# Optimization experiments

Measured on AMD Instinct MI355X. Metric: run time of the kernel, lower is better.

## Reference

```python
import jax, jax.numpy as jnp
import numpy as np
from jax import lax

B, C1, C2, OUT, H, W = 8, 256, 128, 256, 64, 64
MID = max(C1, C2)
D = max(MID // 8, 4)

def conv1x1(x, w, b=None):
    # x: [B,C,H,W], w: [O,C]
    y = jnp.einsum('bchw,oc->bohw', x, w)
    if b is not None:
        y = y + b[None, :, None, None]
    return y

def dwconv3x3(x, w, b):
    # depthwise 3x3, padding=1; w: [C,1,3,3]
    y = lax.conv_general_dilated(x, w, (1, 1), 'SAME',
                                 dimension_numbers=('NCHW', 'OIHW', 'NCHW'),
                                 feature_group_count=x.shape[1])
    return y + b[None, :, None, None]

def setup_inputs() -> dict:
    key = jax.random.key(0)
    ks = jax.random.split(key, 16)
    def w1x1(k, o, i):
        return jax.random.normal(k, (o, i), jnp.float32) * np.sqrt(2.0 / o)
    def wdw(k, c):
        return jax.random.normal(k, (c, 1, 3, 3), jnp.float32) * np.sqrt(2.0 / (9 * c))
    z = lambda c: jnp.zeros((c,), jnp.float32)
    return {
        'x1': jax.random.normal(ks[0], (B, C1, H, W), jnp.float32),
        'x2': jax.random.normal(ks[1], (B, C2, H, W), jnp.float32),
        'conv_r_w': w1x1(ks[2], MID, C1), 'conv_r_b': z(MID),
        'conv_n_w': w1x1(ks[3], MID, C2), 'conv_n_b': z(MID),
        'mlp_w1': w1x1(ks[4], D, MID),
        'mlp_w2': w1x1(ks[5], 2 * MID, D),
        'pq_w': w1x1(ks[6], MID, MID), 'pq_b': z(MID),
        'dq_w': wdw(ks[7], MID), 'dq_b': z(MID),
        'pk_w': w1x1(ks[8], MID, MID), 'pk_b': z(MID),
        'dk_w': wdw(ks[9], MID), 'dk_b': z(MID),
        'pv_w': w1x1(ks[10], MID, MID), 'pv_b': z(MID),
        'dv_w': wdw(ks[11], MID), 'dv_b': z(MID),
        'out_w': w1x1(ks[12], OUT, MID), 'out_b': z(OUT),
        'alpha': jnp.float32(1.0),
        'lambd': jnp.float32(0.5),
        'beta': jnp.float32(0.5),
    }

def reference(x1, x2, conv_r_w, conv_r_b, conv_n_w, conv_n_b, mlp_w1, mlp_w2,
              pq_w, pq_b, dq_w, dq_b, pk_w, pk_b, dk_w, dk_b,
              pv_w, pv_b, dv_w, dv_b, out_w, out_b, alpha, lambd, beta):
    FR = conv1x1(x1, conv_r_w, conv_r_b)          # [B,C,H,W]
    FN = conv1x1(x2, conv_n_w, conv_n_b)          # [B,C,H,W]
    stack = jnp.stack([FR, FN], axis=1)           # [B,2,C,H,W]
    feats_sum = FR + FN
    pooled = feats_sum.mean(axis=(2, 3))          # [B,C] (adaptive avg pool 1x1)
    h = jax.nn.relu(jnp.einsum('bc,dc->bd', pooled, mlp_w1))
    a = jnp.einsum('bd,ed->be', h, mlp_w2).reshape(B, 2, MID)
    attn = jax.nn.softmax(a, axis=1)              # softmax over the 2 branches
    Fw = jnp.einsum('bkchw,bkc->bchw', stack, attn)
    Q = dwconv3x3(conv1x1(Fw, pq_w, pq_b), dq_w, dq_b)
    K = dwconv3x3(conv1x1(Fw, pk_w, pk_b), dk_w, dk_b)
    V = dwconv3x3(conv1x1(Fw, pv_w, pv_b), dv_w, dv_b)
    FQ = jnp.fft.fft2(Q.astype(jnp.float32), axes=(-2, -1))   # complex64 [B,C,H,W]
    FK = jnp.fft.fft2(K.astype(jnp.float32), axes=(-2, -1))
    elem = (FQ * FK).reshape(B, MID, H * W)                    # [B,C,HW]
    FQf = FQ.reshape(B, MID, H * W)
    FKf = FK.reshape(B, MID, H * W)
    attn_matrix = jnp.einsum('bcn,bdn->bcd', FQf, FKf)         # complex [B,C,C]
    attn_w = jax.nn.softmax(jnp.abs(attn_matrix) / alpha, axis=-1)
    attn_wc = attn_w.astype(jnp.complex64)
    F_CFR = jnp.einsum('bcd,bdn->bcn', attn_wc, elem).reshape(B, MID, H, W)
    cfr = jnp.real(jnp.fft.ifft2(F_CFR, axes=(-2, -1))).astype(Q.dtype)
    F_DFR = V - lambd * V * cfr
    freq_out = Q * cfr + F_DFR
    output = beta * freq_out + (1.0 - beta) * Fw
    return conv1x1(output, out_w, out_b)
```

## Files before the change

kernel.cpp:

```cpp
#include <hip/hip_runtime.h>
#include <math.h>

#ifndef M_PI
#define M_PI 3.14159265358979323846
#endif

typedef unsigned int u32;

constexpr int  NB   = 8;
constexpr int  CH   = 256;
constexpr long HW   = 4096;
constexpr long SLOT = (long)NB * CH * HW;
constexpr int  SPLITK = 8;
constexpr long ST   = (long)CH * HW;

__device__ __forceinline__ float rne_hi(float x) {
  unsigned u = __float_as_uint(x);
  unsigned r = (u + 0x7FFFu + ((u >> 16) & 1u)) & 0xFFFF0000u;
  return __uint_as_float(r);
}
__device__ __forceinline__ u32 packf(float x) {
  const float h = rne_hi(x);
  const float l = x - h;
  return (__float_as_uint(h) & 0xFFFF0000u) | (__float_as_uint(l) >> 16);
}
__device__ __forceinline__ float unpackf(u32 u) {
  return __uint_as_float(u & 0xFFFF0000u) + __uint_as_float(u << 16);
}
__device__ __forceinline__ unsigned bfpair(float x, float y) {
  return (__float_as_uint(x) >> 16) | (__float_as_uint(y) & 0xFFFF0000u);
}

typedef short bf16x8 __attribute__((ext_vector_type(8)));
typedef float f32x4  __attribute__((ext_vector_type(4)));

__global__ __launch_bounds__(256)
void cvt_kernel(const float* __restrict__ src, u32* __restrict__ dst, int n4)
{
  const int i = blockIdx.x * 256 + threadIdx.x;
  if (i < n4) {
    const float4 v = ((const float4*)src)[i];
    uint4 o;
    o.x = packf(v.x); o.y = packf(v.y); o.z = packf(v.z); o.w = packf(v.w);
    ((uint4*)dst)[i] = o;
  }
}

template<bool BPACKED, int EPI>
__global__ __launch_bounds__(256)
void gemm_mfma(const u32* __restrict__ A, const void* __restrict__ Bv,
               void* __restrict__ Cv, const float* __restrict__ bias,
               int K, long aStride, long bStride, long cStride,
               const u32* __restrict__ qb, const u32* __restrict__ vb,
               const u32* __restrict__ fwb,
               const float* __restrict__ lambd, const float* __restrict__ beta)
{
  constexpr int N = 4096;
  __shared__ __align__(16) unsigned short sAh[128 * 48];
  __shared__ __align__(16) unsigned short sAl[128 * 48];
  __shared__ __align__(16) unsigned short sBh[128 * 48];
  __shared__ __align__(16) unsigned short sBl[128 * 48];

  const int tid = threadIdx.x;
  const int b   = blockIdx.z;
  const int m0  = blockIdx.y * 128;
  const int n0  = blockIdx.x * 128;
  const u32* Ab = A + (long)b * aStride;

  const int ar = tid >> 1;
  const int ak = (tid & 1) * 16;
  const int aBase = ar * 48 + ak;
  const int bn = tid & 127;
  const int bk = (tid >> 7) * 16;
  const int bBase = bn * 48 + bk;

  const int wv = tid >> 6, lane = tid & 63;
  const int wy = wv >> 1, wx = wv & 1;
  const int quad = lane >> 4, l15 = lane & 15;

  f32x4 acc[4][4];
#pragma unroll
  for (int i = 0; i < 4; ++i)
#pragma unroll
    for (int j = 0; j < 4; ++j) acc[i][j] = (f32x4){0.f, 0.f, 0.f, 0.f};

  u32   ra[16];
  u32   rbu[16];
  float rbf[16];
  {
    const u32* ap = Ab + (long)(m0 + ar) * K + ak;
#pragma unroll
    for (int i = 0; i < 4; ++i) {
      const uint4 t = *(const uint4*)(ap + i * 4);
      ra[4*i] = t.x; ra[4*i+1] = t.y; ra[4*i+2] = t.z; ra[4*i+3] = t.w;
    }
    if (BPACKED) {
      const u32* bp = (const u32*)Bv + (long)b * bStride + (long)bk * N + n0 + bn;
#pragma unroll
      for (int i = 0; i < 16; ++i) rbu[i] = bp[(long)i * N];
    } else {
      const float* bp = (const float*)Bv + (long)b * bStride + (long)bk * N + n0 + bn;
#pragma unroll
      for (int i = 0; i < 16; ++i) rbf[i] = bp[(long)i * N];
    }
  }

  for (int kt = 0; kt < K; kt += 32) {
    {
      u32 hi[8], lo[8];
#pragma unroll
      for (int e = 0; e < 8; ++e) {
        const u32 u0 = ra[2*e], u1 = ra[2*e+1];
        hi[e] = (u0 >> 16) | (u1 & 0xFFFF0000u);
        lo[e] = (u0 & 0xFFFFu) | (u1 << 16);
      }
      *(uint4*)&sAh[aBase]     = make_uint4(hi[0], hi[1], hi[2], hi[3]);
      *(uint4*)&sAh[aBase + 8] = make_uint4(hi[4], hi[5], hi[6], hi[7]);
      *(uint4*)&sAl[aBase]     = make_uint4(lo[0], lo[1], lo[2], lo[3]);
      *(uint4*)&sAl[aBase + 8] = make_uint4(lo[4], lo[5], lo[6], lo[7]);
    }
    if (BPACKED) {
      u32 hi[8], lo[8];
#pragma unroll
      for (int e = 0; e < 8; ++e) {
        const u32 u0 = rbu[2*e], u1 = rbu[2*e+1];
        hi[e] = (u0 >> 16) | (u1 & 0xFFFF0000u);
        lo[e] = (u0 & 0xFFFFu) | (u1 << 16);
      }
      *(uint4*)&sBh[bBase]     = make_uint4(hi[0], hi[1], hi[2], hi[3]);
      *(uint4*)&sBh[bBase + 8] = make_uint4(hi[4], hi[5], hi[6], hi[7]);
      *(uint4*)&sBl[bBase]     = make_uint4(lo[0], lo[1], lo[2], lo[3]);
      *(uint4*)&sBl[bBase + 8] = make_uint4(lo[4], lo[5], lo[6], lo[7]);
    } else {
      float h[16], l[16];
#pragma unroll
      for (int e = 0; e < 16; ++e) { h[e] = rne_hi(rbf[e]); l[e] = rbf[e] - h[e]; }
      *(uint4*)&sBh[bBase]     = make_uint4(bfpair(h[0],h[1]), bfpair(h[2],h[3]),
                                            bfpair(h[4],h[5]), bfpair(h[6],h[7]));
      *(uint4*)&sBh[bBase + 8] = make_uint4(bfpair(h[8],h[9]), bfpair(h[10],h[11]),
                                            bfpair(h[12],h[13]), bfpair(h[14],h[15]));
      *(uint4*)&sBl[bBase]     = make_uint4(bfpair(l[0],l[1]), bfpair(l[2],l[3]),
                                            bfpair(l[4],l[5]), bfpair(l[6],l[7]));
      *(uint4*)&sBl[bBase + 8] = make_uint4(bfpair(l[8],l[9]), bfpair(l[10],l[11]),
                                            bfpair(l[12],l[13]), bfpair(l[14],l[15]));
    }
    __syncthreads();

    if (kt + 32 < K) {
      const u32* ap = Ab + (long)(m0 + ar) * K + kt + 32 + ak;
#pragma unroll
      for (int i = 0; i < 4; ++i) {
        const uint4 t = *(const uint4*)(ap + i * 4);
        ra[4*i] = t.x; ra[4*i+1] = t.y; ra[4*i+2] = t.z; ra[4*i+3] = t.w;
      }
      if (BPACKED) {
        const u32* bp = (const u32*)Bv + (long)b * bStride + (long)(kt + 32 + bk) * N + n0 + bn;
#pragma unroll
        for (int i = 0; i < 16; ++i) rbu[i] = bp[(long)i * N];
      } else {
        const float* bp = (const float*)Bv + (long)b * bStride + (long)(kt + 32 + bk) * N + n0 + bn;
#pragma unroll
        for (int i = 0; i < 16; ++i) rbf[i] = bp[(long)i * N];
      }
    }

    bf16x8 ah[4], al[4];
#pragma unroll
    for (int i = 0; i < 4; ++i) {
      const int idx = (wy * 64 + i * 16 + l15) * 48 + quad * 8;
      ah[i] = *(const bf16x8*)&sAh[idx];
      al[i] = *(const bf16x8*)&sAl[idx];
    }
#pragma unroll
    for (int j = 0; j < 4; ++j) {
      const int idx = (wx * 64 + j * 16 + l15) * 48 + quad * 8;
      const bf16x8 bh = *(const bf16x8*)&sBh[idx];
      const bf16x8 bl = *(const bf16x8*)&sBl[idx];
#pragma unroll
      for (int i = 0; i < 4; ++i) {
        acc[i][j] = __builtin_amdgcn_mfma_f32_16x16x32_bf16(ah[i], bh, acc[i][j], 0, 0, 0);
        acc[i][j] = __builtin_amdgcn_mfma_f32_16x16x32_bf16(ah[i], bl, acc[i][j], 0, 0, 0);
        acc[i][j] = __builtin_amdgcn_mfma_f32_16x16x32_bf16(al[i], bh, acc[i][j], 0, 0, 0);
      }
    }
    __syncthreads();
  }

  if (EPI == 0) {
    float* Cb = (float*)Cv + (long)b * cStride;
#pragma unroll
    for (int i = 0; i < 4; ++i)
#pragma unroll
      for (int r = 0; r < 4; ++r) {
        const int row = m0 + wy * 64 + i * 16 + quad * 4 + r;
        const float bb = bias ? bias[row] : 0.f;
#pragma unroll
        for (int j = 0; j < 4; ++j) {
          const int col = n0 + wx * 64 + j * 16 + l15;
          Cb[(long)row * N + col] = acc[i][j][r] + bb;
        }
      }
  } else if (EPI == 1) {
    u32* Cb = (u32*)Cv + (long)b * cStride;
#pragma unroll
    for (int i = 0; i < 4; ++i)
#pragma unroll
      for (int r = 0; r < 4; ++r) {
        const int row = m0 + wy * 64 + i * 16 + quad * 4 + r;
        const float bb = bias ? bias[row] : 0.f;
#pragma unroll
        for (int j = 0; j < 4; ++j) {
          const int col = n0 + wx * 64 + j * 16 + l15;
          Cb[(long)row * N + col] = packf(acc[i][j][r] + bb);
        }
      }
  } else {
    u32* Cb = (u32*)Cv + (long)b * cStride;
    const float lam = lambd[0], bet = beta[0];
#pragma unroll
    for (int i = 0; i < 4; ++i)
#pragma unroll
      for (int r = 0; r < 4; ++r) {
        const int row = m0 + wy * 64 + i * 16 + quad * 4 + r;
#pragma unroll
        for (int j = 0; j < 4; ++j) {
          const int col = n0 + wx * 64 + j * 16 + l15;
          const long off = (long)row * N + col;
          const long gi  = (long)b * cStride + off;
          const float q = unpackf(qb[gi]);
          const float v = unpackf(vb[gi]);
          const float f = unpackf(fwb[gi]);
          Cb[off] = packf(bet * (acc[i][j][r] * (q - lam * v) + v) + (1.f - bet) * f);
        }
      }
  }
}

__global__ __launch_bounds__(256)
void gemm_logits(const u32* __restrict__ Q, const u32* __restrict__ Kr,
                 float* __restrict__ Lp)
{
  __shared__ __align__(16) unsigned short sAh[128 * 48];
  __shared__ __align__(16) unsigned short sAl[128 * 48];
  __shared__ __align__(16) unsigned short sBh[128 * 48];
  __shared__ __align__(16) unsigned short sBl[128 * 48];

  const int tid = threadIdx.x;
  const int bz  = blockIdx.z;
  const int b   = bz >> 3, sp = bz & 7;
  const int m0  = blockIdx.y * 128;
  const int n0  = blockIdx.x * 128;
  const long k0b = (long)sp * 512;

  const int ar = tid >> 1;
  const int ak = (tid & 1) * 16;
  const int aBase = ar * 48 + ak;

  const int wv = tid >> 6, lane = tid & 63;
  const int wy = wv >> 1, wx = wv & 1;
  const int quad = lane >> 4, l15 = lane & 15;

  f32x4 acc[4][4];
#pragma unroll
  for (int i = 0; i < 4; ++i)
#pragma unroll
    for (int j = 0; j < 4; ++j) acc[i][j] = (f32x4){0.f, 0.f, 0.f, 0.f};

  const u32* Abase = Q  + (long)b * ST + (long)(m0 + ar) * 4096 + k0b + ak;
  const u32* Bbase = Kr + (long)b * ST + (long)(n0 + ar) * 4096 + k0b + ak;

  u32 ra[16], rb[16];
#pragma unroll
  for (int i = 0; i < 4; ++i) {
    uint4 t = *(const uint4*)(Abase + i * 4);
    ra[4*i] = t.x; ra[4*i+1] = t.y; ra[4*i+2] = t.z; ra[4*i+3] = t.w;
    t = *(const uint4*)(Bbase + i * 4);
    rb[4*i] = t.x; rb[4*i+1] = t.y; rb[4*i+2] = t.z; rb[4*i+3] = t.w;
  }

  for (int kt = 0; kt < 512; kt += 32) {
    {
      u32 hi[8], lo[8];
#pragma unroll
      for (int e = 0; e < 8; ++e) {
        const u32 u0 = ra[2*e], u1 = ra[2*e+1];
        hi[e] = (u0 >> 16) | (u1 & 0xFFFF0000u);
        lo[e] = (u0 & 0xFFFFu) | (u1 << 16);
      }
      *(uint4*)&sAh[aBase]     = make_uint4(hi[0], hi[1], hi[2], hi[3]);
      *(uint4*)&sAh[aBase + 8] = make_uint4(hi[4], hi[5], hi[6], hi[7]);
      *(uint4*)&sAl[aBase]     = make_uint4(lo[0], lo[1], lo[2], lo[3]);
      *(uint4*)&sAl[aBase + 8] = make_uint4(lo[4], lo[5], lo[6], lo[7]);
#pragma unroll
      for (int e = 0; e < 8; ++e) {
        const u32 u0 = rb[2*e], u1 = rb[2*e+1];
        hi[e] = (u0 >> 16) | (u1 & 0xFFFF0000u);
        lo[e] = (u0 & 0xFFFFu) | (u1 << 16);
      }
      *(uint4*)&sBh[aBase]     = make_uint4(hi[0], hi[1], hi[2], hi[3]);
      *(uint4*)&sBh[aBase + 8] = make_uint4(hi[4], hi[5], hi[6], hi[7]);
      *(uint4*)&sBl[aBase]     = make_uint4(lo[0], lo[1], lo[2], lo[3]);
      *(uint4*)&sBl[aBase + 8] = make_uint4(lo[4], lo[5], lo[6], lo[7]);
    }
    __syncthreads();

    if (kt + 32 < 512) {
#pragma unroll
      for (int i = 0; i < 4; ++i) {
        uint4 t = *(const uint4*)(Abase + kt + 32 + i * 4);
        ra[4*i] = t.x; ra[4*i+1] = t.y; ra[4*i+2] = t.z; ra[4*i+3] = t.w;
        t = *(const uint4*)(Bbase + kt + 32 + i * 4);
        rb[4*i] = t.x; rb[4*i+1] = t.y; rb[4*i+2] = t.z; rb[4*i+3] = t.w;
      }
    }

    bf16x8 ah[4], al[4];
#pragma unroll
    for (int i = 0; i < 4; ++i) {
      const int idx = (wy * 64 + i * 16 + l15) * 48 + quad * 8;
      ah[i] = *(const bf16x8*)&sAh[idx];
      al[i] = *(const bf16x8*)&sAl[idx];
    }
#pragma unroll
    for (int j = 0; j < 4; ++j) {
      const int idx = (wx * 64 + j * 16 + l15) * 48 + quad * 8;
      const bf16x8 bh = *(const bf16x8*)&sBh[idx];
      const bf16x8 bl = *(const bf16x8*)&sBl[idx];
#pragma unroll
      for (int i = 0; i < 4; ++i) {
        acc[i][j] = __builtin_amdgcn_mfma_f32_16x16x32_bf16(ah[i], bh, acc[i][j], 0, 0, 0);
        acc[i][j] = __builtin_amdgcn_mfma_f32_16x16x32_bf16(ah[i], bl, acc[i][j], 0, 0, 0);
        acc[i][j] = __builtin_amdgcn_mfma_f32_16x16x32_bf16(al[i], bh, acc[i][j], 0, 0, 0);
      }
    }
    __syncthreads();
  }

  float* Lb = Lp + (long)bz * 65536;
#pragma unroll
  for (int i = 0; i < 4; ++i)
#pragma unroll
    for (int r = 0; r < 4; ++r) {
      const int row = m0 + wy * 64 + i * 16 + quad * 4 + r;
#pragma unroll
      for (int j = 0; j < 4; ++j) {
        const int col = n0 + wx * 64 + j * 16 + l15;
        Lb[(long)row * 256 + col] = acc[i][j][r];
      }
    }
}

__global__ __launch_bounds__(256)
void pool_kernel(const u32* __restrict__ FR, const u32* __restrict__ FN,
                 float* __restrict__ pooled)
{
  __shared__ float red[256];
  const int bc = blockIdx.x, tid = threadIdx.x;
  const uint4* a = (const uint4*)(FR + (long)bc * HW);
  const uint4* b = (const uint4*)(FN + (long)bc * HW);
  float s = 0.f;
  for (int v = tid; v < 1024; v += 256) {
    const uint4 x = a[v];
    s += unpackf(x.x) + unpackf(x.y) + unpackf(x.z) + unpackf(x.w);
    const uint4 y = b[v];
    s += unpackf(y.x) + unpackf(y.y) + unpackf(y.z) + unpackf(y.w);
  }
  red[tid] = s; __syncthreads();
  for (int o = 128; o > 0; o >>= 1) {
    if (tid < o) red[tid] += red[tid + o];
    __syncthreads();
  }
  if (tid == 0) pooled[bc] = red[0] * (1.f / 4096.f);
}

__global__ __launch_bounds__(256)
void attn2_kernel(const float* __restrict__ pooled, const float* __restrict__ w1,
                  const float* __restrict__ w2, float* __restrict__ attn2)
{
  __shared__ float ps[256];
  __shared__ float hs[32];
  const int b = blockIdx.x, tid = threadIdx.x;
  ps[tid] = pooled[b * 256 + tid];
  __syncthreads();
  if (tid < 32) {
    float a = 0.f;
    for (int c = 0; c < 256; ++c) a += ps[c] * w1[tid * 256 + c];
    hs[tid] = fmaxf(a, 0.f);
  }
  __syncthreads();
  float a0 = 0.f, a1 = 0.f;
  for (int d = 0; d < 32; ++d) {
    const float h = hs[d];
    a0 += h * w2[tid * 32 + d];
    a1 += h * w2[(256 + tid) * 32 + d];
  }
  const float m  = fmaxf(a0, a1);
  const float e0 = expf(a0 - m), e1 = expf(a1 - m);
  const float inv = 1.f / (e0 + e1);
  attn2[b * 512 + tid]       = e0 * inv;
  attn2[b * 512 + 256 + tid] = e1 * inv;
}

__global__ __launch_bounds__(256)
void fw_kernel(const u32* __restrict__ FR, const u32* __restrict__ FN,
               const float* __restrict__ attn2, u32* __restrict__ FW)
{
  const int b = blockIdx.z, c = blockIdx.y;
  const float a0 = attn2[b * 512 + c];
  const float a1 = attn2[b * 512 + 256 + c];
  const long base4 = ((long)b * 256 + c) * 1024;
  const int i = blockIdx.x * 256 + threadIdx.x;
  const uint4 r = ((const uint4*)FR)[base4 + i];
  const uint4 n = ((const uint4*)FN)[base4 + i];
  uint4 o;
  o.x = packf(a0 * unpackf(r.x) + a1 * unpackf(n.x));
  o.y = packf(a0 * unpackf(r.y) + a1 * unpackf(n.y));
  o.z = packf(a0 * unpackf(r.z) + a1 * unpackf(n.z));
  o.w = packf(a0 * unpackf(r.w) + a1 * unpackf(n.w));
  ((uint4*)FW)[base4 + i] = o;
}

__global__ __launch_bounds__(256)
void dw_kernel(const u32* __restrict__ in, const float* __restrict__ w,
               const float* __restrict__ bias, u32* __restrict__ out,
               u32* __restrict__ out_rev)
{
  __shared__ float img[66][66];
  const int bc = blockIdx.x, tid = threadIdx.x;
  const int c = bc & 255;
  for (int v = tid; v < 66 * 66; v += 256) ((float*)img)[v] = 0.f;
  __syncthreads();
  const uint4* in4 = (const uint4*)(in + (long)bc * HW);
  for (int v = tid; v < 1024; v += 256) {
    const uint4 x = in4[v];
    const int r = v >> 4, c0 = ((v & 15) << 2) + 1;
    img[r + 1][c0 + 0] = unpackf(x.x);
    img[r + 1][c0 + 1] = unpackf(x.y);
    img[r + 1][c0 + 2] = unpackf(x.z);
    img[r + 1][c0 + 3] = unpackf(x.w);
  }
  float wr[9];
#pragma unroll
  for (int j = 0; j < 9; ++j) wr[j] = w[c * 9 + j];
  const float bb = bias[c];
  __syncthreads();
  for (int p = tid; p < 4096; p += 256) {
    const int y = p >> 6, x = p & 63;
    float s = bb;
#pragma unroll
    for (int ky = 0; ky < 3; ++ky)
#pragma unroll
      for (int kx = 0; kx < 3; ++kx)
        s = fmaf(wr[ky * 3 + kx], img[y + ky][x + kx], s);
    const u32 u = packf(s);
    out[(long)bc * HW + p] = u;
    if (out_rev)
      out_rev[(long)bc * HW + (((64 - y) & 63) << 6) + ((64 - x) & 63)] = u;
  }
}

#define SWA(r, c) (((r) << 6) | ((c) ^ (r)))
#define REV6(x)   ((((x) & 3) << 4) | ((x) & 12) | ((x) >> 4))

__device__ __forceinline__ float2 cmul(float2 a, float2 w) {
  return make_float2(a.x * w.x - a.y * w.y, a.x * w.y + a.y * w.x);
}
__device__ __forceinline__ float2 cmulc(float2 a, float2 w) {
  return make_float2(a.x * w.x + a.y * w.y, a.y * w.x - a.x * w.y);
}
__device__ __forceinline__ void r4fwd(float2& x0, float2& x1, float2& x2, float2& x3) {
  const float2 t0 = make_float2(x0.x + x2.x, x0.y + x2.y);
  const float2 t1 = make_float2(x0.x - x2.x, x0.y - x2.y);
  const float2 t2 = make_float2(x1.x + x3.x, x1.y + x3.y);
  const float2 t3 = make_float2(x1.x - x3.x, x1.y - x3.y);
  x0 = make_float2(t0.x + t2.x, t0.y + t2.y);
  x2 = make_float2(t0.x - t2.x, t0.y - t2.y);
  x1 = make_float2(t1.x + t3.y, t1.y - t3.x);
  x3 = make_float2(t1.x - t3.y, t1.y + t3.x);
}
__device__ __forceinline__ void r4inv(float2& x0, float2& x1, float2& x2, float2& x3) {
  const float2 t0 = make_float2(x0.x + x2.x, x0.y + x2.y);
  const float2 t1 = make_float2(x0.x - x2.x, x0.y - x2.y);
  const float2 t2 = make_float2(x1.x + x3.x, x1.y + x3.y);
  const float2 t3 = make_float2(x1.x - x3.x, x1.y - x3.y);
  x0 = make_float2(t0.x + t2.x, t0.y + t2.y);
  x2 = make_float2(t0.x - t2.x, t0.y - t2.y);
  x1 = make_float2(t1.x - t3.y, t1.y + t3.x);
  x3 = make_float2(t1.x + t3.y, t1.y - t3.x);
}

__device__ __forceinline__ void fft_fwd(float2* __restrict__ Z,
                                        const float2 (&wA)[3][3],
                                        const float2 (&wB)[4][3],
                                        int lane, int kb)
{
  for (int pass = 0; pass < 2; ++pass) {
    {
      float2 x[16];
#pragma unroll
      for (int m = 0; m < 16; ++m) {
        const int p = 16 * kb + m;
        x[m] = Z[pass ? SWA(p, lane) : SWA(lane, p)];
      }
#pragma unroll
      for (int c = 0; c < 4; ++c)
        r4fwd(x[4*c], x[4*c+1], x[4*c+2], x[4*c+3]);
#pragma unroll
      for (int j = 0; j < 4; ++j) {
        if (j) {
          x[j+4]  = cmul(x[j+4],  wA[j-1][0]);
          x[j+8]  = cmul(x[j+8],  wA[j-1][1]);
          x[j+12] = cmul(x[j+12], wA[j-1][2]);
        }
        r4fwd(x[j], x[j+4], x[j+8], x[j+12]);
      }
#pragma unroll
      for (int m = 0; m < 16; ++m) {
        const int p = 16 * kb + m;
        Z[pass ? SWA(p, lane) : SWA(lane, p)] = x[m];
      }
    }
    __syncthreads();
#pragma unroll
    for (int q = 0; q < 4; ++q) {
      const int k = kb + 4 * q;
      const int a0 = pass ? SWA(k,      lane) : SWA(lane, k);
      const int a1 = pass ? SWA(k + 16, lane) : SWA(lane, k + 16);
      const int a2 = pass ? SWA(k + 32, lane) : SWA(lane, k + 32);
      const int a3 = pass ? SWA(k + 48, lane) : SWA(lane, k + 48);
      float2 x0 = Z[a0], x1 = Z[a1], x2 = Z[a2], x3 = Z[a3];
      x1 = cmul(x1, wB[q][0]);
      x2 = cmul(x2, wB[q][1]);
      x3 = cmul(x3, wB[q][2]);
      r4fwd(x0, x1, x2, x3);
      Z[a0] = x0; Z[a1] = x1; Z[a2] = x2; Z[a3] = x3;
    }
    __syncthreads();
  }
}

__device__ __forceinline__ void fft_inv(float2* __restrict__ Z,
                                        const float2 (&wA)[3][3],
                                        const float2 (&wB)[4][3],
                                        int lane, int kb)
{
  for (int pass = 0; pass < 2; ++pass) {
#pragma unroll
    for (int q = 0; q < 4; ++q) {
      const int k = kb + 4 * q;
      const int a0 = pass ? SWA(lane, k)      : SWA(k,      lane);
      const int a1 = pass ? SWA(lane, k + 16) : SWA(k + 16, lane);
      const int a2 = pass ? SWA(lane, k + 32) : SWA(k + 32, lane);
      const int a3 = pass ? SWA(lane, k + 48) : SWA(k + 48, lane);
      float2 x0 = Z[a0], x1 = Z[a1], x2 = Z[a2], x3 = Z[a3];
      r4inv(x0, x1, x2, x3);
      x1 = cmulc(x1, wB[q][0]);
      x2 = cmulc(x2, wB[q][1]);
      x3 = cmulc(x3, wB[q][2]);
      Z[a0] = x0; Z[a1] = x1; Z[a2] = x2; Z[a3] = x3;
    }
    __syncthreads();
    {
      float2 x[16];
#pragma unroll
      for (int m = 0; m < 16; ++m) {
        const int p = 16 * kb + m;
        x[m] = Z[pass ? SWA(lane, p) : SWA(p, lane)];
      }
#pragma unroll
      for (int j = 0; j < 4; ++j) {
        r4inv(x[j], x[j+4], x[j+8], x[j+12]);
        if (j) {
          x[j+4]  = cmulc(x[j+4],  wA[j-1][0]);
          x[j+8]  = cmulc(x[j+8],  wA[j-1][1]);
          x[j+12] = cmulc(x[j+12], wA[j-1][2]);
        }
      }
#pragma unroll
      for (int c = 0; c < 4; ++c)
        r4inv(x[4*c], x[4*c+1], x[4*c+2], x[4*c+3]);
#pragma unroll
      for (int m = 0; m < 16; ++m) {
        const int p = 16 * kb + m;
        Z[pass ? SWA(lane, p) : SWA(p, lane)] = x[m];
      }
    }
    __syncthreads();
  }
}

__global__ __launch_bounds__(256, 3)
void sconv_kernel(const u32* __restrict__ Qg, const u32* __restrict__ Kg,
                  u32* __restrict__ Sg)
{
  __shared__ float2 Z[4096];
  __shared__ float2 twt[64];
  const int tid = threadIdx.x;
  const int lane = tid & 63;
  const int kb   = tid >> 6;
  const long base = (long)blockIdx.x * 4096;
  if (tid < 64) {
    float sn, cs;
    __sincosf(-2.f * (float)M_PI * (float)tid * (1.f / 64.f), &sn, &cs);
    twt[tid] = make_float2(cs, sn);
  }

  {
    const uint4* Q4 = (const uint4*)(Qg + base);
    const uint4* K4 = (const uint4*)(Kg + base);
#pragma unroll
    for (int i = 0; i < 4; ++i) {
      const int v = tid + 256 * i;
      const uint4 q = Q4[v], k = K4[v];
      const int r = v >> 4, w = v & 15;
      const int R  = REV6(r);
      const int cb = ((w & 3) << 2) | (w >> 2);
      Z[SWA(R, cb)]      = make_float2(unpackf(q.x), unpackf(k.x));
      Z[SWA(R, cb + 16)] = make_float2(unpackf(q.y), unpackf(k.y));
      Z[SWA(R, cb + 32)] = make_float2(unpackf(q.z), unpackf(k.z));
      Z[SWA(R, cb + 48)] = make_float2(unpackf(q.w), unpackf(k.w));
    }
  }
  __syncthreads();

  float2 wA[3][3], wB[4][3];
#pragma unroll
  for (int j = 1; j < 4; ++j) {
    wA[j-1][0] = twt[(4  * j) & 63];
    wA[j-1][1] = twt[(8  * j) & 63];
    wA[j-1][2] = twt[(12 * j) & 63];
  }
#pragma unroll
  for (int q = 0; q < 4; ++q) {
    const int k = kb + 4 * q;
    wB[q][0] = twt[k];
    wB[q][1] = twt[(2 * k) & 63];
    wB[q][2] = twt[(3 * k) & 63];
  }

  fft_fwd(Z, wA, wB, lane, kb);

#pragma unroll
  for (int i = 0; i < 9; ++i) {
    const int n = tid + 256 * i;
    if (n < 2112) {
      const int u = n >> 6, vv = n & 63;
      if (!((u == 0 || u == 32) && vv > 32)) {
        const int u2 = (64 - u) & 63, v2 = (64 - vv) & 63;
        const int az = SWA(u, vv), am = SWA(u2, v2);
        const float2 z = Z[az];
        const float2 m = Z[am];
        const float dre = 0.25f * (z.x * z.x - z.y * z.y - m.x * m.x + m.y * m.y);
        const float dim = 0.5f  * (z.x * z.y + m.x * m.y);
        Z[az] = make_float2(dim, -dre);
        Z[am] = make_float2(dim,  dre);
      }
    }
  }
  __syncthreads();

  fft_inv(Z, wA, wB, lane, kb);

  uint4* S4 = (uint4*)(Sg + base);
#pragma unroll
  for (int i = 0; i < 4; ++i) {
    const int v = tid + 256 * i;
    const int y = v >> 4, w = v & 15;
    const int Rr = REV6(y);
    const int cb = ((w & 3) << 2) | (w >> 2);
    uint4 o;
    o.x = packf(Z[SWA(Rr, cb)].x      * (1.f / 4096.f));
    o.y = packf(Z[SWA(Rr, cb + 16)].x * (1.f / 4096.f));
    o.z = packf(Z[SWA(Rr, cb + 32)].x * (1.f / 4096.f));
    o.w = packf(Z[SWA(Rr, cb + 48)].x * (1.f / 4096.f));
    S4[v] = o;
  }
}

__global__ __launch_bounds__(256)
void softmax_kernel(const float* __restrict__ Lp, u32* __restrict__ L,
                    const float* __restrict__ alpha)
{
  __shared__ float red[256];
  const int row = blockIdx.x, tid = threadIdx.x;
  const int b = row >> 8, c = row & 255;
  const float sc = 4096.f / alpha[0];
  float acc = 0.f;
#pragma unroll
  for (int s = 0; s < SPLITK; ++s)
    acc += Lp[((long)(b * SPLITK + s) * 65536) + (long)c * 256 + tid];
  const float v = fabsf(acc) * sc;
  red[tid] = v; __syncthreads();
  for (int o = 128; o > 0; o >>= 1) {
    if (tid < o) red[tid] = fmaxf(red[tid], red[tid + o]);
    __syncthreads();
  }
  const float mx = red[0];
  __syncthreads();
  const float e = expf(v - mx);
  red[tid] = e; __syncthreads();
  for (int o = 128; o > 0; o >>= 1) {
    if (tid < o) red[tid] += red[tid + o];
    __syncthreads();
  }
  L[(long)row * 256 + tid] = packf(e / red[0]);
}

extern "C" void kernel_launch(void* const* d_in, const int* in_sizes, int n_in,
                              void* d_out, int out_size, void* d_ws, size_t ws_size,
                              hipStream_t stream)
{
  const float* x1       = (const float*)d_in[0];
  const float* x2       = (const float*)d_in[1];
  const float* conv_r_w = (const float*)d_in[2];
  const float* conv_r_b = (const float*)d_in[3];
  const float* conv_n_w = (const float*)d_in[4];
  const float* conv_n_b = (const float*)d_in[5];
  const float* mlp_w1   = (const float*)d_in[6];
  const float* mlp_w2   = (const float*)d_in[7];
  const float* pq_w     = (const float*)d_in[8];
  const float* pq_b     = (const float*)d_in[9];
  const float* dq_w     = (const float*)d_in[10];
  const float* dq_b     = (const float*)d_in[11];
  const float* pk_w     = (const float*)d_in[12];
  const float* pk_b     = (const float*)d_in[13];
  const float* dk_w     = (const float*)d_in[14];
  const float* dk_b     = (const float*)d_in[15];
  const float* pv_w     = (const float*)d_in[16];
  const float* pv_b     = (const float*)d_in[17];
  const float* dv_w     = (const float*)d_in[18];
  const float* dv_b     = (const float*)d_in[19];
  const float* out_w    = (const float*)d_in[20];
  const float* out_b    = (const float*)d_in[21];
  const float* alpha    = (const float*)d_in[22];
  const float* lambd    = (const float*)d_in[23];
  const float* beta     = (const float*)d_in[24];

  u32* s = (u32*)d_ws;
  u32* S0 = s;
  u32* S1 = s + SLOT;
  u32* S2 = s + 2 * SLOT;
  u32* S3 = s + 3 * SLOT;
  u32* S4 = s + 4 * SLOT;
  u32* S5 = s + 5 * SLOT;
  float* Lp     = (float*)(s + 6 * SLOT);
  u32*   Lb     = (u32*)(Lp + (long)8 * SPLITK * 65536);
  float* pooled = (float*)(Lb + (long)8 * 65536);
  float* attn2  = pooled + 2048;
  u32*   wR     = (u32*)(attn2 + 4096);
  u32*   wN     = wR + 65536;
  u32*   wQ     = wN + 32768;
  u32*   wK     = wQ + 65536;
  u32*   wV     = wK + 65536;
  u32*   wO     = wV + 65536;

  const size_t needed =
      (size_t)(6 * SLOT + (long)8 * SPLITK * 65536 + 8L * 65536 + 2048 + 4096
               + 65536 * 5 + 32768) * 4;
  if (ws_size < needed) return;

  const long ST2 = (long)128 * HW;
  const long STL = (long)256 * 256;
  const dim3 gBig(32, 2, 8);

  cvt_kernel<<<64, 256, 0, stream>>>(conv_r_w, wR, 16384);
  cvt_kernel<<<32, 256, 0, stream>>>(conv_n_w, wN, 8192);
  cvt_kernel<<<64, 256, 0, stream>>>(pq_w, wQ, 16384);
  cvt_kernel<<<64, 256, 0, stream>>>(pk_w, wK, 16384);
  cvt_kernel<<<64, 256, 0, stream>>>(pv_w, wV, 16384);
  cvt_kernel<<<64, 256, 0, stream>>>(out_w, wO, 16384);

  gemm_mfma<false, 1><<<gBig, 256, 0, stream>>>(wR, x1, S0, conv_r_b,
      256, 0L, ST, ST, nullptr, nullptr, nullptr, nullptr, nullptr);
  gemm_mfma<false, 1><<<gBig, 256, 0, stream>>>(wN, x2, S1, conv_n_b,
      128, 0L, ST2, ST, nullptr, nullptr, nullptr, nullptr, nullptr);

  pool_kernel<<<2048, 256, 0, stream>>>(S0, S1, pooled);
  attn2_kernel<<<8, 256, 0, stream>>>(pooled, mlp_w1, mlp_w2, attn2);
  fw_kernel<<<dim3(4, 256, 8), 256, 0, stream>>>(S0, S1, attn2, S2);

  gemm_mfma<true, 1><<<gBig, 256, 0, stream>>>(wQ, S2, S3, pq_b,
      256, 0L, ST, ST, nullptr, nullptr, nullptr, nullptr, nullptr);
  gemm_mfma<true, 1><<<gBig, 256, 0, stream>>>(wK, S2, S4, pk_b,
      256, 0L, ST, ST, nullptr, nullptr, nullptr, nullptr, nullptr);
  gemm_mfma<true, 1><<<gBig, 256, 0, stream>>>(wV, S2, S5, pv_b,
      256, 0L, ST, ST, nullptr, nullptr, nullptr, nullptr, nullptr);

  dw_kernel<<<2048, 256, 0, stream>>>(S3, dq_w, dq_b, S0, nullptr);
  dw_kernel<<<2048, 256, 0, stream>>>(S4, dk_w, dk_b, S1, S3);
  dw_kernel<<<2048, 256, 0, stream>>>(S5, dv_w, dv_b, S4, nullptr);

  sconv_kernel<<<2048, 256, 0, stream>>>(S0, S1, S5);

  gemm_logits<<<dim3(2, 2, 64), 256, 0, stream>>>(S0, S3, Lp);
  softmax_kernel<<<2048, 256, 0, stream>>>(Lp, Lb, alpha);

  gemm_mfma<true, 2><<<gBig, 256, 0, stream>>>(Lb, S5, S2, nullptr,
      256, STL, ST, ST, S0, S4, S2, lambd, beta);

  gemm_mfma<true, 0><<<gBig, 256, 0, stream>>>(wO, S2, d_out, out_b,
      256, 0L, ST, ST, nullptr, nullptr, nullptr, nullptr, nullptr);
}
```

Before: 448.1 us.

## Process two channels per block, sharing one inverse FFT via real/imag packing

Each sconv block now handles two channel planes: it runs the forward FFTs on both, then packs the two real-valued products into the real and imaginary parts of a single spectrum. One inverse FFT then yields both outputs, cutting inverse FFT work in half. Twiddle factors are now computed in registers or hardcoded instead of going through a shared table. Shared memory per block doubles to 64KB, so occupancy drops (launch bounds 3 to 2) and the grid is halved.

```diff
diff --git a/kernel.cpp b/kernel.cpp
--- a/kernel.cpp
+++ b/kernel.cpp
@@ -489,156 +489,168 @@
   x3 = make_float2(t1.x + t3.y, t1.y - t3.x);
 }
 
-__device__ __forceinline__ void fft_fwd(float2* __restrict__ Z,
-                                        const float2 (&wA)[3][3],
-                                        const float2 (&wB)[4][3],
-                                        int lane, int kb)
-{
-  for (int pass = 0; pass < 2; ++pass) {
-    {
-      float2 x[16];
-#pragma unroll
-      for (int m = 0; m < 16; ++m) {
-        const int p = 16 * kb + m;
-        x[m] = Z[pass ? SWA(p, lane) : SWA(lane, p)];
-      }
-#pragma unroll
-      for (int c = 0; c < 4; ++c)
-        r4fwd(x[4*c], x[4*c+1], x[4*c+2], x[4*c+3]);
-#pragma unroll
-      for (int j = 0; j < 4; ++j) {
-        if (j) {
-          x[j+4]  = cmul(x[j+4],  wA[j-1][0]);
-          x[j+8]  = cmul(x[j+8],  wA[j-1][1]);
-          x[j+12] = cmul(x[j+12], wA[j-1][2]);
-        }
-        r4fwd(x[j], x[j+4], x[j+8], x[j+12]);
-      }
-#pragma unroll
-      for (int m = 0; m < 16; ++m) {
-        const int p = 16 * kb + m;
-        Z[pass ? SWA(p, lane) : SWA(lane, p)] = x[m];
-      }
-    }
-    __syncthreads();
-#pragma unroll
-    for (int q = 0; q < 4; ++q) {
-      const int k = kb + 4 * q;
-      const int a0 = pass ? SWA(k,      lane) : SWA(lane, k);
-      const int a1 = pass ? SWA(k + 16, lane) : SWA(lane, k + 16);
-      const int a2 = pass ? SWA(k + 32, lane) : SWA(lane, k + 32);
-      const int a3 = pass ? SWA(k + 48, lane) : SWA(lane, k + 48);
-      float2 x0 = Z[a0], x1 = Z[a1], x2 = Z[a2], x3 = Z[a3];
-      x1 = cmul(x1, wB[q][0]);
-      x2 = cmul(x2, wB[q][1]);
-      x3 = cmul(x3, wB[q][2]);
-      r4fwd(x0, x1, x2, x3);
-      Z[a0] = x0; Z[a1] = x1; Z[a2] = x2; Z[a3] = x3;
-    }
-    __syncthreads();
-  }
-}
-
-__device__ __forceinline__ void fft_inv(float2* __restrict__ Z,
-                                        const float2 (&wA)[3][3],
-                                        const float2 (&wB)[4][3],
-                                        int lane, int kb)
-{
-  for (int pass = 0; pass < 2; ++pass) {
-#pragma unroll
-    for (int q = 0; q < 4; ++q) {
-      const int k = kb + 4 * q;
-      const int a0 = pass ? SWA(lane, k)      : SWA(k,      lane);
-      const int a1 = pass ? SWA(lane, k + 16) : SWA(k + 16, lane);
-      const int a2 = pass ? SWA(lane, k + 32) : SWA(k + 32, lane);
-      const int a3 = pass ? SWA(lane, k + 48) : SWA(k + 48, lane);
-      float2 x0 = Z[a0], x1 = Z[a1], x2 = Z[a2], x3 = Z[a3];
-      r4inv(x0, x1, x2, x3);
-      x1 = cmulc(x1, wB[q][0]);
-      x2 = cmulc(x2, wB[q][1]);
-      x3 = cmulc(x3, wB[q][2]);
-      Z[a0] = x0; Z[a1] = x1; Z[a2] = x2; Z[a3] = x3;
-    }
-    __syncthreads();
-    {
-      float2 x[16];
-#pragma unroll
-      for (int m = 0; m < 16; ++m) {
-        const int p = 16 * kb + m;
-        x[m] = Z[pass ? SWA(lane, p) : SWA(p, lane)];
-      }
-#pragma unroll
-      for (int j = 0; j < 4; ++j) {
-        r4inv(x[j], x[j+4], x[j+8], x[j+12]);
-        if (j) {
-          x[j+4]  = cmulc(x[j+4],  wA[j-1][0]);
-          x[j+8]  = cmulc(x[j+8],  wA[j-1][1]);
-          x[j+12] = cmulc(x[j+12], wA[j-1][2]);
-        }
-      }
-#pragma unroll
-      for (int c = 0; c < 4; ++c)
-        r4inv(x[4*c], x[4*c+1], x[4*c+2], x[4*c+3]);
-#pragma unroll
-      for (int m = 0; m < 16; ++m) {
-        const int p = 16 * kb + m;
-        Z[pass ? SWA(lane, p) : SWA(p, lane)] = x[m];
-      }
-    }
-    __syncthreads();
-  }
-}
-
-__global__ __launch_bounds__(256, 3)
+__device__ __forceinline__ void fused01_fwd(float2* __restrict__ Z,
+                                            const float2 (&wA)[3][3],
+                                            int lane, int kb, int pass)
+{
+  float2 x[16];
+#pragma unroll
+  for (int m = 0; m < 16; ++m) {
+    const int p = 16 * kb + m;
+    x[m] = Z[pass ? SWA(p, lane) : SWA(lane, p)];
+  }
+#pragma unroll
+  for (int c = 0; c < 4; ++c)
+    r4fwd(x[4*c], x[4*c+1], x[4*c+2], x[4*c+3]);
+#pragma unroll
+  for (int j = 0; j < 4; ++j) {
+    if (j) {
+      x[j+4]  = cmul(x[j+4],  wA[j-1][0]);
+      x[j+8]  = cmul(x[j+8],  wA[j-1][1]);
+      x[j+12] = cmul(x[j+12], wA[j-1][2]);
+    }
+    r4fwd(x[j], x[j+4], x[j+8], x[j+12]);
+  }
+#pragma unroll
+  for (int m = 0; m < 16; ++m) {
+    const int p = 16 * kb + m;
+    Z[pass ? SWA(p, lane) : SWA(lane, p)] = x[m];
+  }
+}
+
+__device__ __forceinline__ void stage2_fwd(float2* __restrict__ Z,
+                                           const float2 (&wB)[4][3],
+                                           int lane, int kb, int pass)
+{
+#pragma unroll
+  for (int q = 0; q < 4; ++q) {
+    const int k = kb + 4 * q;
+    const int a0 = pass ? SWA(k,      lane) : SWA(lane, k);
+    const int a1 = pass ? SWA(k + 16, lane) : SWA(lane, k + 16);
+    const int a2 = pass ? SWA(k + 32, lane) : SWA(lane, k + 32);
+    const int a3 = pass ? SWA(k + 48, lane) : SWA(lane, k + 48);
+    float2 x0 = Z[a0], x1 = Z[a1], x2 = Z[a2], x3 = Z[a3];
+    x1 = cmul(x1, wB[q][0]);
+    x2 = cmul(x2, wB[q][1]);
+    x3 = cmul(x3, wB[q][2]);
+    r4fwd(x0, x1, x2, x3);
+    Z[a0] = x0; Z[a1] = x1; Z[a2] = x2; Z[a3] = x3;
+  }
+}
+
+__device__ __forceinline__ void stage2_inv(float2* __restrict__ Z,
+                                           const float2 (&wB)[4][3],
+                                           int lane, int kb, int pass)
+{
+#pragma unroll
+  for (int q = 0; q < 4; ++q) {
+    const int k = kb + 4 * q;
+    const int a0 = pass ? SWA(lane, k)      : SWA(k,      lane);
+    const int a1 = pass ? SWA(lane, k + 16) : SWA(k + 16, lane);
+    const int a2 = pass ? SWA(lane, k + 32) : SWA(k + 32, lane);
+    const int a3 = pass ? SWA(lane, k + 48) : SWA(k + 48, lane);
+    float2 x0 = Z[a0], x1 = Z[a1], x2 = Z[a2], x3 = Z[a3];
+    r4inv(x0, x1, x2, x3);
+    x1 = cmulc(x1, wB[q][0]);
+    x2 = cmulc(x2, wB[q][1]);
+    x3 = cmulc(x3, wB[q][2]);
+    Z[a0] = x0; Z[a1] = x1; Z[a2] = x2; Z[a3] = x3;
+  }
+}
+
+__device__ __forceinline__ void fused01_inv(float2* __restrict__ Z,
+                                            const float2 (&wA)[3][3],
+                                            int lane, int kb, int pass)
+{
+  float2 x[16];
+#pragma unroll
+  for (int m = 0; m < 16; ++m) {
+    const int p = 16 * kb + m;
+    x[m] = Z[pass ? SWA(lane, p) : SWA(p, lane)];
+  }
+#pragma unroll
+  for (int j = 0; j < 4; ++j) {
+    r4inv(x[j], x[j+4], x[j+8], x[j+12]);
+    if (j) {
+      x[j+4]  = cmulc(x[j+4],  wA[j-1][0]);
+      x[j+8]  = cmulc(x[j+8],  wA[j-1][1]);
+      x[j+12] = cmulc(x[j+12], wA[j-1][2]);
+    }
+  }
+#pragma unroll
+  for (int c = 0; c < 4; ++c)
+    r4inv(x[4*c], x[4*c+1], x[4*c+2], x[4*c+3]);
+#pragma unroll
+  for (int m = 0; m < 16; ++m) {
+    const int p = 16 * kb + m;
+    Z[pass ? SWA(lane, p) : SWA(p, lane)] = x[m];
+  }
+}
+
+__device__ __forceinline__ void sconv_load(float2* __restrict__ Z,
+                                           const u32* __restrict__ Qg,
+                                           const u32* __restrict__ Kg,
+                                           long base, int tid)
+{
+  const uint4* Q4 = (const uint4*)(Qg + base);
+  const uint4* K4 = (const uint4*)(Kg + base);
+#pragma unroll
+  for (int i = 0; i < 4; ++i) {
+    const int v = tid + 256 * i;
+    const uint4 q = Q4[v], k = K4[v];
+    const int r = v >> 4, w = v & 15;
+    const int R  = REV6(r);
+    const int cb = ((w & 3) << 2) | (w >> 2);
+    Z[SWA(R, cb)]      = make_float2(unpackf(q.x), unpackf(k.x));
+    Z[SWA(R, cb + 16)] = make_float2(unpackf(q.y), unpackf(k.y));
+    Z[SWA(R, cb + 32)] = make_float2(unpackf(q.z), unpackf(k.z));
+    Z[SWA(R, cb + 48)] = make_float2(unpackf(q.w), unpackf(k.w));
+  }
+}
+
+__global__ __launch_bounds__(256, 2)
 void sconv_kernel(const u32* __restrict__ Qg, const u32* __restrict__ Kg,
                   u32* __restrict__ Sg)
 {
-  __shared__ float2 Z[4096];
-  __shared__ float2 twt[64];
-  const int tid = threadIdx.x;
+  __shared__ float2 ZA[4096];
+  __shared__ float2 ZB[4096];
+  const int tid  = threadIdx.x;
   const int lane = tid & 63;
   const int kb   = tid >> 6;
-  const long base = (long)blockIdx.x * 4096;
-  if (tid < 64) {
+  const long base = (long)blockIdx.x * 8192;
+
+  const float2 wA[3][3] = {
+    { make_float2( 0.92387953251f, -0.38268343236f),
+      make_float2( 0.70710678119f, -0.70710678119f),
+      make_float2( 0.38268343236f, -0.92387953251f) },
+    { make_float2( 0.70710678119f, -0.70710678119f),
+      make_float2( 0.f,            -1.f),
+      make_float2(-0.70710678119f, -0.70710678119f) },
+    { make_float2( 0.38268343236f, -0.92387953251f),
+      make_float2(-0.70710678119f, -0.70710678119f),
+      make_float2(-0.92387953251f,  0.38268343236f) } };
+  float2 wB[4][3];
+#pragma unroll
+  for (int q = 0; q < 4; ++q) {
+    const float k = (float)(kb + 4 * q);
     float sn, cs;
-    __sincosf(-2.f * (float)M_PI * (float)tid * (1.f / 64.f), &sn, &cs);
-    twt[tid] = make_float2(cs, sn);
-  }
-
-  {
-    const uint4* Q4 = (const uint4*)(Qg + base);
-    const uint4* K4 = (const uint4*)(Kg + base);
-#pragma unroll
-    for (int i = 0; i < 4; ++i) {
-      const int v = tid + 256 * i;
-      const uint4 q = Q4[v], k = K4[v];
-      const int r = v >> 4, w = v & 15;
-      const int R  = REV6(r);
-      const int cb = ((w & 3) << 2) | (w >> 2);
-      Z[SWA(R, cb)]      = make_float2(unpackf(q.x), unpackf(k.x));
-      Z[SWA(R, cb + 16)] = make_float2(unpackf(q.y), unpackf(k.y));
-      Z[SWA(R, cb + 32)] = make_float2(unpackf(q.z), unpackf(k.z));
-      Z[SWA(R, cb + 48)] = make_float2(unpackf(q.w), unpackf(k.w));
-    }
-  }
+    __sincosf(-2.f * (float)M_PI * (1.f / 64.f) * k,        &sn, &cs); wB[q][0] = make_float2(cs, sn);
+    __sincosf(-2.f * (float)M_PI * (1.f / 64.f) * (2.f*k),  &sn, &cs); wB[q][1] = make_float2(cs, sn);
+    __sincosf(-2.f * (float)M_PI * (1.f / 64.f) * (3.f*k),  &sn, &cs); wB[q][2] = make_float2(cs, sn);
+  }
+
+  sconv_load(ZA, Qg, Kg, base, tid);
+  sconv_load(ZB, Qg, Kg, base + 4096, tid);
   __syncthreads();
 
-  float2 wA[3][3], wB[4][3];
-#pragma unroll
-  for (int j = 1; j < 4; ++j) {
-    wA[j-1][0] = twt[(4  * j) & 63];
-    wA[j-1][1] = twt[(8  * j) & 63];
-    wA[j-1][2] = twt[(12 * j) & 63];
-  }
-#pragma unroll
-  for (int q = 0; q < 4; ++q) {
-    const int k = kb + 4 * q;
-    wB[q][0] = twt[k];
-    wB[q][1] = twt[(2 * k) & 63];
-    wB[q][2] = twt[(3 * k) & 63];
-  }
-
-  fft_fwd(Z, wA, wB, lane, kb);
+  for (int pass = 0; pass < 2; ++pass) {
+    fused01_fwd(ZA, wA, lane, kb, pass);
+    fused01_fwd(ZB, wA, lane, kb, pass);
+    __syncthreads();
+    stage2_fwd(ZA, wB, lane, kb, pass);
+    stage2_fwd(ZB, wB, lane, kb, pass);
+    __syncthreads();
+  }
 
 #pragma unroll
   for (int i = 0; i < 9; ++i) {
@@ -648,32 +660,49 @@
       if (!((u == 0 || u == 32) && vv > 32)) {
         const int u2 = (64 - u) & 63, v2 = (64 - vv) & 63;
         const int az = SWA(u, vv), am = SWA(u2, v2);
-        const float2 z = Z[az];
-        const float2 m = Z[am];
-        const float dre = 0.25f * (z.x * z.x - z.y * z.y - m.x * m.x + m.y * m.y);
-        const float dim = 0.5f  * (z.x * z.y + m.x * m.y);
-        Z[az] = make_float2(dim, -dre);
-        Z[am] = make_float2(dim,  dre);
+        const float2 z0 = ZA[az], m0 = ZA[am];
+        const float2 z1 = ZB[az], m1 = ZB[am];
+        const float dre0 = 0.25f * (z0.x*z0.x - z0.y*z0.y - m0.x*m0.x + m0.y*m0.y);
+        const float dim0 = 0.5f  * (z0.x*z0.y + m0.x*m0.y);
+        const float dre1 = 0.25f * (z1.x*z1.x - z1.y*z1.y - m1.x*m1.x + m1.y*m1.y);
+        const float dim1 = 0.5f  * (z1.x*z1.y + m1.x*m1.y);
+        ZA[az] = make_float2(dim0 + dre1, dim1 - dre0);
+        ZA[am] = make_float2(dim0 - dre1, dim1 + dre0);
       }
     }
   }
   __syncthreads();
 
-  fft_inv(Z, wA, wB, lane, kb);
-
-  uint4* S4 = (uint4*)(Sg + base);
+  for (int pass = 0; pass < 2; ++pass) {
+    stage2_inv(ZA, wB, lane, kb, pass);
+    __syncthreads();
+    fused01_inv(ZA, wA, lane, kb, pass);
+    __syncthreads();
+  }
+
+  uint4* Sa = (uint4*)(Sg + base);
+  uint4* Sb = (uint4*)(Sg + base + 4096);
 #pragma unroll
   for (int i = 0; i < 4; ++i) {
     const int v = tid + 256 * i;
     const int y = v >> 4, w = v & 15;
     const int Rr = REV6(y);
     const int cb = ((w & 3) << 2) | (w >> 2);
+    const float2 e0 = ZA[SWA(Rr, cb)];
+    const float2 e1 = ZA[SWA(Rr, cb + 16)];
+    const float2 e2 = ZA[SWA(Rr, cb + 32)];
+    const float2 e3 = ZA[SWA(Rr, cb + 48)];
     uint4 o;
-    o.x = packf(Z[SWA(Rr, cb)].x      * (1.f / 4096.f));
-    o.y = packf(Z[SWA(Rr, cb + 16)].x * (1.f / 4096.f));
-    o.z = packf(Z[SWA(Rr, cb + 32)].x * (1.f / 4096.f));
-    o.w = packf(Z[SWA(Rr, cb + 48)].x * (1.f / 4096.f));
-    S4[v] = o;
+    o.x = packf(e0.x * (1.f / 4096.f));
+    o.y = packf(e1.x * (1.f / 4096.f));
+    o.z = packf(e2.x * (1.f / 4096.f));
+    o.w = packf(e3.x * (1.f / 4096.f));
+    Sa[v] = o;
+    o.x = packf(e0.y * (1.f / 4096.f));
+    o.y = packf(e1.y * (1.f / 4096.f));
+    o.z = packf(e2.y * (1.f / 4096.f));
+    o.w = packf(e3.y * (1.f / 4096.f));
+    Sb[v] = o;
   }
 }
 
@@ -790,7 +819,7 @@
   dw_kernel<<<2048, 256, 0, stream>>>(S4, dk_w, dk_b, S1, S3);
   dw_kernel<<<2048, 256, 0, stream>>>(S5, dv_w, dv_b, S4, nullptr);
 
-  sconv_kernel<<<2048, 256, 0, stream>>>(S0, S1, S5);
+  sconv_kernel<<<1024, 256, 0, stream>>>(S0, S1, S5);
 
   gemm_logits<<<dim3(2, 2, 64), 256, 0, stream>>>(S0, S3, Lp);
   softmax_kernel<<<2048, 256, 0, stream>>>(Lp, Lb, alpha);
```

New measurement: 446.7 us. Within noise of the previous version (-0.3%).
